# Performance work log

Hardware: AMD Instinct MI355X
Metric: run time of the kernel (lower is better)

The kernel has to match this reference:

```python
import jax, jax.numpy as jnp
import numpy as np

NUM_ITERS = 3

def squash(t, axis):
    # scale = |t|^2/(1+|t|^2); out = scale * t / |t|
    sn = jnp.sum(t * t, axis=axis, keepdims=True)
    return (sn / (1.0 + sn)) * t / jnp.sqrt(sn)


def setup_inputs() -> dict:
    key = jax.random.key(0)
    k1, k2, k3, k4 = jax.random.split(key, 4)
    B = 128
    inputs = jax.random.normal(k1, (B, 256, 20, 20), dtype=jnp.float32)
    conv_w = jax.random.normal(k2, (8, 32, 256, 9, 9), dtype=jnp.float32) * 0.05
    conv_b = jax.random.normal(k3, (8, 32), dtype=jnp.float32) * 0.05
    route_weights = jax.random.normal(k4, (10, 1152, 8, 16), dtype=jnp.float32)
    return {"inputs": inputs, "conv_w": conv_w, "conv_b": conv_b,
            "route_weights": route_weights}


def reference(inputs, conv_w, conv_b, route_weights):
    B = inputs.shape[0]
    K, O, Cin, kh, kw = conv_w.shape          # 8 capsules, 32 out-chans each
    # --- primary capsules: 8 parallel convs fused into one grouped-output conv ---
    w = conv_w.reshape(K * O, Cin, kh, kw)
    out = jax.lax.conv_general_dilated(
        inputs, w, window_strides=(2, 2), padding='VALID',
        dimension_numbers=('NCHW', 'OIHW', 'NCHW'))  # [B, K*O, 6, 6]
    out = out + conv_b.reshape(K * O)[None, :, None, None]
    H = out.shape[-1]
    x = out.reshape(B, K, O * H * H).transpose(0, 2, 1)  # [B, 1152, 8]
    x = squash(x, axis=2)
    # --- routing layer ---
    # prediction_vectors: x[None,:,:,None,:] @ W[:,None,:,:,:] -> [10,B,1152,1,16]
    pred = jnp.einsum('bri,crio->cbro', x, route_weights)[:, :, :, None, :]
    logits = jnp.zeros_like(pred)
    v = None
    for i in range(NUM_ITERS):
        # routing_softmax(dim=2): softmax over the routes axis (faithful to source)
        c = jax.nn.softmax(logits, axis=2)
        s = jnp.sum(c * pred, axis=2, keepdims=True)  # [10,B,1,1,16]
        v = squash(s, axis=1)                          # squash default dim=1 (batch) -- faithful
        if i != NUM_ITERS - 1:
            logits = logits + jnp.sum(pred * v, axis=-1, keepdims=True)
    # [10,B,1,1,16] -> squeeze -> [10,B,16] -> permute(1,0,2) -> [B,10,16]
    return jnp.squeeze(v).transpose(1, 0, 2)
```

## Files before the change

kernel.cpp:

```cpp
#include <hip/hip_runtime.h>
#include <math.h>

typedef _Float16 f16;
typedef _Float16 f16x4 __attribute__((ext_vector_type(4)));
typedef _Float16 f16x8 __attribute__((ext_vector_type(8)));
typedef float f32x4 __attribute__((ext_vector_type(4)));
typedef float f32x8 __attribute__((ext_vector_type(8)));

#define AS1 __attribute__((address_space(1)))
#define AS3 __attribute__((address_space(3)))

__device__ __forceinline__ void gld_lds16(const f16* g, f16* l) {
#if defined(__has_builtin) && __has_builtin(__builtin_amdgcn_global_load_lds)
    __builtin_amdgcn_global_load_lds((const AS1 void*)g, (AS3 void*)l, 16, 0, 0);
#else
    *(uint4*)l = *(const uint4*)g;
#endif
}

__global__ __launch_bounds__(256) void transpose_input(
    const float* __restrict__ inp, f16* __restrict__ out)
{
    const int b = blockIdx.x, c0 = blockIdx.y * 32, p0 = blockIdx.z * 32;
    const int tx = threadIdx.x, ty = threadIdx.y;
    __shared__ float t[32][33];
#pragma unroll
    for (int j = 0; j < 4; ++j) {
        int c = ty + j * 8, p = p0 + tx;
        if (p < 400) t[c][tx] = inp[((size_t)b * 256 + c0 + c) * 400 + p];
    }
    __syncthreads();
#pragma unroll
    for (int j = 0; j < 4; ++j) {
        int p = p0 + ty + j * 8;
        if (p < 400) out[((size_t)b * 400 + p) * 256 + c0 + tx] = (f16)t[tx][ty + j * 8];
    }
}

__global__ __launch_bounds__(256) void permute_w(
    const float* __restrict__ cw, f16* __restrict__ w_t)
{
    const int n = blockIdx.x, t = threadIdx.x;
    __shared__ f16 buf[81 * 258];
    const float* src = cw + (size_t)n * 20736;
    for (int i = t; i < 20736; i += 256) {
        int cin = i / 81, p = i - cin * 81;
        buf[p * 258 + cin] = (f16)src[i];
    }
    __syncthreads();
    f16* dst = w_t + (size_t)n * 20736;
    for (int j = t; j < 20736; j += 256) {
        int p = j >> 8, cin = j & 255;
        dst[j] = buf[p * 258 + cin];
    }
}

__global__ __launch_bounds__(256) void permute_rw(
    const float* __restrict__ rw, f16* __restrict__ rwh)
{
    int g = blockIdx.x * 256 + threadIdx.x;
    int cr = g >> 5, rem = g & 31;
    int o = rem >> 1, h = (rem & 1) * 4;
    const float* src = rw + (size_t)cr * 128 + o;
    f16x4 v;
#pragma unroll
    for (int j = 0; j < 4; ++j) v[j] = (f16)src[(h + j) * 16];
    *(f16x4*)(rwh + (size_t)cr * 128 + o * 8 + h) = v;
}

#define SPLITK 14
__global__ __launch_bounds__(256, 2) void conv_mfma(
    const f16* __restrict__ in_t,
    const f16* __restrict__ w_t,
    f16* __restrict__ part)
{
    __shared__ f16 As[3][128 * 32];
    __shared__ f16 Bs[3][256 * 32];
    const int tid = threadIdx.x;
    const int lane = tid & 63, wave = tid >> 6;
    const int wm = wave >> 1, wn = wave & 1;

    const int bid = blockIdx.x + 36 * blockIdx.z;
    const int wgid = (bid & 7) * 63 + (bid >> 3);
    const int m0 = (wgid % 36) * 128;
    const int kz = wgid / 36;

    const int kc0 = kz * 46 + (kz < 4 ? kz : 4);
    const int NT  = (kz < 4) ? 47 : 46;

    int srcA[2], srcB[4];
#pragma unroll
    for (int i = 0; i < 2; ++i) {
        int pairp = i * 32 + (tid >> 3);
        int chunk8 = (tid & 7) ^ (pairp & 7);
        int e = chunk8 >> 2, q4 = chunk8 & 3;
        int m = m0 + pairp * 2 + e;
        int b = m / 36, hw = m - b * 36;
        int ho = hw / 6, wo = hw - ho * 6;
        srcA[i] = ((b * 20 + 2 * ho) * 20 + 2 * wo) * 256 + q4 * 8;
    }
#pragma unroll
    for (int i = 0; i < 4; ++i) {
        int pairp = i * 32 + (tid >> 3);
        int chunk8 = (tid & 7) ^ (pairp & 7);
        int e = chunk8 >> 2, q4 = chunk8 & 3;
        int n = pairp * 2 + e;
        srcB[i] = n * 20736 + q4 * 8;
    }

    const int row = lane & 15, quad = lane >> 4;
    int offA[4], offB[8];
#pragma unroll
    for (int mt = 0; mt < 4; ++mt) {
        int m = wm * 64 + mt * 16 + row;
        int ph8 = (((m & 1) << 2) + quad) ^ ((m >> 1) & 7);
        offA[mt] = (m >> 1) * 64 + ph8 * 8;
    }
#pragma unroll
    for (int nt = 0; nt < 8; ++nt) {
        int n = wn * 128 + nt * 16 + row;
        int ph8 = (((n & 1) << 2) + quad) ^ ((n >> 1) & 7);
        offB[nt] = (n >> 1) * 64 + ph8 * 8;
    }

    f32x4 acc[4][8] = {};

#define KOFFS(T) int kc = kc0 + (T); int pp = kc >> 3, cq = kc & 7;           \
    int kh = pp / 9, kw = pp - kh * 9;                                        \
    int koffA = (kh * 20 + kw) * 256 + cq * 32; int koffB = kc * 32;
#define STAGE1(T, BUF) do { KOFFS(T)                                          \
        gld_lds16(in_t + srcA[0] + koffA, &As[BUF][tid * 8]);                 \
        gld_lds16(in_t + srcA[1] + koffA, &As[BUF][2048 + tid * 8]);          \
        gld_lds16(w_t + srcB[0] + koffB, &Bs[BUF][tid * 8]);                  \
    } while (0)
#define STAGE2(T, BUF) do { KOFFS(T)                                          \
        gld_lds16(w_t + srcB[1] + koffB, &Bs[BUF][2048 + tid * 8]);           \
        gld_lds16(w_t + srcB[2] + koffB, &Bs[BUF][4096 + tid * 8]);           \
        gld_lds16(w_t + srcB[3] + koffB, &Bs[BUF][6144 + tid * 8]);           \
    } while (0)

    STAGE1(0, 0); STAGE2(0, 0);
    STAGE1(1, 1); STAGE2(1, 1);
    asm volatile("s_waitcnt vmcnt(6)" ::: "memory");
    __builtin_amdgcn_s_barrier();

    int buf = 0;
    for (int t = 0; t < NT; ++t) {
        const f16* Ab = &As[buf][0];
        const f16* Bb = &Bs[buf][0];
        int bn = buf + 2; if (bn >= 3) bn -= 3;
        f16x8 af[4], bfr[8];

#pragma unroll
        for (int mt = 0; mt < 4; ++mt) af[mt] = *(const f16x8*)(Ab + offA[mt]);
#pragma unroll
        for (int nt = 0; nt < 4; ++nt) bfr[nt] = *(const f16x8*)(Bb + offB[nt]);
        if (t + 2 < NT) STAGE1(t + 2, bn);
        __builtin_amdgcn_s_barrier();
        asm volatile("s_waitcnt lgkmcnt(0)" ::: "memory");
        __builtin_amdgcn_sched_barrier(0);
        __builtin_amdgcn_s_setprio(1);
#pragma unroll
        for (int mt = 0; mt < 4; ++mt)
#pragma unroll
            for (int nt = 0; nt < 4; ++nt)
                acc[mt][nt] = __builtin_amdgcn_mfma_f32_16x16x32_f16(
                    af[mt], bfr[nt], acc[mt][nt], 0, 0, 0);
        __builtin_amdgcn_s_setprio(0);
        __builtin_amdgcn_s_barrier();

#pragma unroll
        for (int nt = 4; nt < 8; ++nt) bfr[nt] = *(const f16x8*)(Bb + offB[nt]);
        if (t + 2 < NT) STAGE2(t + 2, bn);
        if (t + 2 < NT)
            asm volatile("s_waitcnt vmcnt(6)" ::: "memory");
        else if (t + 1 < NT)
            asm volatile("s_waitcnt vmcnt(0)" ::: "memory");
        __builtin_amdgcn_s_barrier();
        asm volatile("s_waitcnt lgkmcnt(0)" ::: "memory");
        __builtin_amdgcn_sched_barrier(0);
        __builtin_amdgcn_s_setprio(1);
#pragma unroll
        for (int mt = 0; mt < 4; ++mt)
#pragma unroll
            for (int nt = 4; nt < 8; ++nt)
                acc[mt][nt] = __builtin_amdgcn_mfma_f32_16x16x32_f16(
                    af[mt], bfr[nt], acc[mt][nt], 0, 0, 0);
        __builtin_amdgcn_s_setprio(0);
        __builtin_amdgcn_s_barrier();

        if (++buf == 3) buf = 0;
    }
#undef STAGE1
#undef STAGE2
#undef KOFFS

    const int col = lane & 15, qr = (lane >> 4) * 4;
    f16* pb = part + (size_t)kz * 4608 * 256;
#pragma unroll
    for (int mt = 0; mt < 4; ++mt)
#pragma unroll
        for (int rg = 0; rg < 4; ++rg) {
            int m = m0 + wm * 64 + mt * 16 + qr + rg;
#pragma unroll
            for (int nt = 0; nt < 8; ++nt) {
                int n = wn * 128 + nt * 16 + col;
                pb[(size_t)m * 256 + n] = (f16)acc[mt][nt][rg];
            }
        }
}

__global__ __launch_bounds__(256) void combine_squash(
    const f16* __restrict__ part, const float* __restrict__ bias,
    f16* __restrict__ xh)
{
    int idx = blockIdx.x * 256 + threadIdx.x;
    int m = idx >> 3, g = idx & 7;
    int b = m / 36, hw = m - b * 36;
    float val[8][4];
#pragma unroll
    for (int k = 0; k < 8; ++k)
#pragma unroll
        for (int j = 0; j < 4; ++j) val[k][j] = bias[k * 32 + g * 4 + j];
#pragma unroll
    for (int s = 0; s < SPLITK; ++s) {
        const f16* p = part + ((size_t)s * 4608 + m) * 256 + g * 4;
#pragma unroll
        for (int k = 0; k < 8; ++k) {
            f16x4 v = *(const f16x4*)(p + k * 32);
#pragma unroll
            for (int j = 0; j < 4; ++j) val[k][j] += (float)v[j];
        }
    }
#pragma unroll
    for (int j = 0; j < 4; ++j) {
        float sn = 0.f;
#pragma unroll
        for (int k = 0; k < 8; ++k) sn += val[k][j] * val[k][j];
        float scale = sqrtf(sn) / (1.f + sn);
        int r = (g * 4 + j) * 36 + hw;
        f16x8 hv;
#pragma unroll
        for (int k = 0; k < 8; ++k) hv[k] = (f16)(val[k][j] * scale);
        *(f16x8*)(xh + ((size_t)b * 1152 + r) * 8) = hv;
    }
}

__global__ __launch_bounds__(256) void pred_s0h(
    const f16* __restrict__ xh,
    const f16* __restrict__ rwh,
    f16* __restrict__ pred,
    float* __restrict__ s0)
{
    const int c = blockIdx.x, r0 = blockIdx.y * 32, b0 = blockIdx.z * 32;
    const int tid = threadIdx.x;
    const int o = tid & 15, rp = tid >> 4;
    const int r = r0 + rp * 2;

    __shared__ float s_sh[32 * 16];
    s_sh[tid] = 0.f; s_sh[tid + 256] = 0.f;

    f16x8 w0h = *(const f16x8*)(rwh + ((size_t)(c * 1152 + r) * 16 + o) * 8);
    f16x8 w1h = *(const f16x8*)(rwh + ((size_t)(c * 1152 + r + 1) * 16 + o) * 8);
    f32x8 W0 = __builtin_convertvector(w0h, f32x8);
    f32x8 W1 = __builtin_convertvector(w1h, f32x8);
    __syncthreads();

    for (int bb = 0; bb < 32; ++bb) {
        const int b = b0 + bb;
        f16x8 x0h = *(const f16x8*)(xh + ((size_t)b * 1152 + r) * 8);
        f16x8 x1h = *(const f16x8*)(xh + ((size_t)b * 1152 + r + 1) * 8);
        f32x8 X0 = __builtin_convertvector(x0h, f32x8);
        f32x8 X1 = __builtin_convertvector(x1h, f32x8);
        float p0 = X0[0]*W0[0] + X0[1]*W0[1] + X0[2]*W0[2] + X0[3]*W0[3]
                 + X0[4]*W0[4] + X0[5]*W0[5] + X0[6]*W0[6] + X0[7]*W0[7];
        float p1 = X1[0]*W1[0] + X1[1]*W1[1] + X1[2]*W1[2] + X1[3]*W1[3]
                 + X1[4]*W1[4] + X1[5]*W1[5] + X1[6]*W1[6] + X1[7]*W1[7];
        f16* pb = pred + ((size_t)(c * 128 + b) * 1152 + r) * 16 + o;
        pb[0]  = (f16)p0;
        pb[16] = (f16)p1;
        float ps = p0 + p1;
        ps += __shfl_xor(ps, 16);
        ps += __shfl_xor(ps, 32);
        if ((tid & 63) < 16) atomicAdd(&s_sh[bb * 16 + o], ps);
    }
    __syncthreads();
    for (int i = tid; i < 512; i += 256) {
        int bb = i >> 4, oo = i & 15;
        atomicAdd(&s0[((size_t)c * 128 + b0 + bb) * 16 + oo], s_sh[i]);
    }
}

__global__ __launch_bounds__(256) void route_f16v(
    const f16* __restrict__ pred,
    const float* __restrict__ sa, const float* __restrict__ za,
    const float* __restrict__ sb2, const float* __restrict__ zb2,
    float* __restrict__ s_out,
    float* __restrict__ z_out)
{
    const int c = blockIdx.x, b = blockIdx.y, tid = threadIdx.x;
    const size_t base = (size_t)(c * 128 + b) * 1152;
    const int o = tid & 15, seg = tid >> 4;

    __shared__ float lred[16][17];
    __shared__ float vs[16];

#define VSADD(S, Z) do {                                                      \
        float part_ = 0.f;                                                    \
        _Pragma("unroll")                                                     \
        for (int j = 0; j < 8; ++j) {                                         \
            int bb = seg * 8 + j;                                             \
            float zin = (Z) ? 1.f / (Z)[c * 128 + bb] : (1.f / 1152.f);       \
            float q = (S)[((size_t)c * 128 + bb) * 16 + o] * zin;             \
            part_ += q * q;                                                   \
        }                                                                     \
        lred[seg][o] = part_;                                                 \
        __syncthreads();                                                      \
        if (tid < 16) {                                                       \
            float t_ = 0.f;                                                   \
            _Pragma("unroll")                                                 \
            for (int i = 0; i < 16; ++i) t_ += lred[i][tid];                  \
            float zin = (Z) ? 1.f / (Z)[c * 128 + b] : (1.f / 1152.f);        \
            vs[tid] += (S)[((size_t)c * 128 + b) * 16 + tid] * zin *          \
                       sqrtf(t_) / (1.f + t_);                                \
        }                                                                     \
        __syncthreads();                                                      \
    } while (0)

    if (tid < 16) vs[tid] = 0.f;
    __syncthreads();
    VSADD(sa, za);
    if (sb2) VSADD(sb2, zb2);
#undef VSADD

    float vr[16];
#pragma unroll
    for (int j = 0; j < 16; ++j) vr[j] = vs[j];

    float sacc[16];
#pragma unroll
    for (int j = 0; j < 16; ++j) sacc[j] = 0.f;
    float zacc = 0.f;

    for (int r = tid; r < 1152; r += 256) {
        const f16x8* pp = (const f16x8*)(pred + (base + r) * 16);
        f32x8 q0 = __builtin_convertvector(pp[0], f32x8);
        f32x8 q1 = __builtin_convertvector(pp[1], f32x8);
        float t = 0.f;
#pragma unroll
        for (int j = 0; j < 8; ++j) t += q0[j] * vr[j] + q1[j] * vr[j + 8];
        float e = __expf(t);
#pragma unroll
        for (int j = 0; j < 8; ++j) { sacc[j] += e * q0[j]; sacc[j + 8] += e * q1[j]; }
        zacc += e;
    }

    __shared__ float red[256][16];
    __shared__ float red2[16][16];
    __shared__ float zred[256];
    __shared__ float zpart[16];
#pragma unroll
    for (int j = 0; j < 16; ++j) red[tid][j] = sacc[j];
    zred[tid] = zacc;
    __syncthreads();
    {
        float t = 0.f;
#pragma unroll
        for (int j = 0; j < 16; ++j) t += red[seg * 16 + j][o];
        red2[seg][o] = t;
        if (tid < 16) {
            float tz = 0.f;
#pragma unroll
            for (int j = 0; j < 16; ++j) tz += zred[tid * 16 + j];
            zpart[tid] = tz;
        }
    }
    __syncthreads();
    if (tid < 16) {
        float t = 0.f;
#pragma unroll
        for (int sg = 0; sg < 16; ++sg) t += red2[sg][tid];
        s_out[(size_t)(c * 128 + b) * 16 + tid] = t;
    } else if (tid == 16) {
        float tz = 0.f;
#pragma unroll
        for (int j = 0; j < 16; ++j) tz += zpart[j];
        z_out[c * 128 + b] = tz;
    }
}

__global__ __launch_bounds__(128) void squash_final(
    const float* __restrict__ s, const float* __restrict__ z,
    float* __restrict__ out)
{
    const int c = blockIdx.x, b = threadIdx.x;
    float sv[16];
    const float* sp = s + ((size_t)c * 128 + b) * 16;
    float zin = 1.f / z[c * 128 + b];
#pragma unroll
    for (int o = 0; o < 16; ++o) sv[o] = sp[o] * zin;
    __shared__ float m[16][129];
#pragma unroll
    for (int o = 0; o < 16; ++o) m[o][b] = sv[o] * sv[o];
    __syncthreads();
    __shared__ float sn[16];
    if (b < 16) {
        float t = 0.f;
        for (int i = 0; i < 128; ++i) t += m[b][i];
        sn[b] = t;
    }
    __syncthreads();
#pragma unroll
    for (int o = 0; o < 16; ++o) {
        float scale = sqrtf(sn[o]) / (1.f + sn[o]);
        out[((size_t)b * 10 + c) * 16 + o] = sv[o] * scale;
    }
}

extern "C" void kernel_launch(void* const* d_in, const int* in_sizes, int n_in,
                              void* d_out, int out_size, void* d_ws, size_t ws_size,
                              hipStream_t stream)
{
    (void)in_sizes; (void)n_in; (void)out_size; (void)ws_size;
    const float* inp = (const float*)d_in[0];
    const float* cw  = (const float*)d_in[1];
    const float* cb  = (const float*)d_in[2];
    const float* rw  = (const float*)d_in[3];
    float* out = (float*)d_out;

    char* ws = (char*)d_ws;
    f16*   part = (f16*)(ws);
    f16*   pred = (f16*)(ws);
    f16*   in_t = (f16*)(ws + 33030144);
    f16*   w_t  = (f16*)(ws + 59244544);
    f16*   rwh  = (f16*)(ws + 69861376);
    f16*   xh   = (f16*)(ws + 72810496);
    float* s0   = (float*)(ws + 75169792);
    float* sB   = (float*)(ws + 75251712);
    float* sC   = (float*)(ws + 75333632);
    float* zB   = (float*)(ws + 75415552);
    float* zC   = (float*)(ws + 75420672);

    hipMemsetAsync(s0, 0, 81920, stream);

    transpose_input<<<dim3(128, 8, 13), dim3(32, 8), 0, stream>>>(inp, in_t);
    permute_w<<<256, 256, 0, stream>>>(cw, w_t);
    permute_rw<<<1440, 256, 0, stream>>>(rw, rwh);
    conv_mfma<<<dim3(36, 1, SPLITK), 256, 0, stream>>>(in_t, w_t, part);
    combine_squash<<<144, 256, 0, stream>>>(part, cb, xh);

    pred_s0h<<<dim3(10, 36, 4), 256, 0, stream>>>(xh, rwh, pred, s0);

    route_f16v<<<dim3(10, 128), 256, 0, stream>>>(pred, s0, nullptr, nullptr, nullptr,
                                                  sB, zB);
    route_f16v<<<dim3(10, 128), 256, 0, stream>>>(pred, s0, nullptr, sB, zB,
                                                  sC, zC);
    squash_final<<<10, 128, 0, stream>>>(sC, zC, out);
}
```

Baseline: 241.0 us.

## Merge preprocessing kernels and memset into one launch, parallelize split-K combine

```diff
diff --git a/kernel.cpp b/kernel.cpp
--- a/kernel.cpp
+++ b/kernel.cpp
@@ -18,54 +18,57 @@
 #endif
 }
 
-__global__ __launch_bounds__(256) void transpose_input(
-    const float* __restrict__ inp, f16* __restrict__ out)
-{
-    const int b = blockIdx.x, c0 = blockIdx.y * 32, p0 = blockIdx.z * 32;
-    const int tx = threadIdx.x, ty = threadIdx.y;
-    __shared__ float t[32][33];
-#pragma unroll
-    for (int j = 0; j < 4; ++j) {
-        int c = ty + j * 8, p = p0 + tx;
-        if (p < 400) t[c][tx] = inp[((size_t)b * 256 + c0 + c) * 400 + p];
-    }
-    __syncthreads();
-#pragma unroll
-    for (int j = 0; j < 4; ++j) {
-        int p = p0 + ty + j * 8;
-        if (p < 400) out[((size_t)b * 400 + p) * 256 + c0 + tx] = (f16)t[tx][ty + j * 8];
-    }
-}
-
-__global__ __launch_bounds__(256) void permute_w(
-    const float* __restrict__ cw, f16* __restrict__ w_t)
-{
-    const int n = blockIdx.x, t = threadIdx.x;
-    __shared__ f16 buf[81 * 258];
-    const float* src = cw + (size_t)n * 20736;
-    for (int i = t; i < 20736; i += 256) {
-        int cin = i / 81, p = i - cin * 81;
-        buf[p * 258 + cin] = (f16)src[i];
-    }
-    __syncthreads();
-    f16* dst = w_t + (size_t)n * 20736;
-    for (int j = t; j < 20736; j += 256) {
-        int p = j >> 8, cin = j & 255;
-        dst[j] = buf[p * 258 + cin];
-    }
-}
-
-__global__ __launch_bounds__(256) void permute_rw(
-    const float* __restrict__ rw, f16* __restrict__ rwh)
-{
-    int g = blockIdx.x * 256 + threadIdx.x;
-    int cr = g >> 5, rem = g & 31;
-    int o = rem >> 1, h = (rem & 1) * 4;
-    const float* src = rw + (size_t)cr * 128 + o;
-    f16x4 v;
-#pragma unroll
-    for (int j = 0; j < 4; ++j) v[j] = (f16)src[(h + j) * 16];
-    *(f16x4*)(rwh + (size_t)cr * 128 + o * 8 + h) = v;
+__global__ __launch_bounds__(256) void mega_pre(
+    const float* __restrict__ inp, f16* __restrict__ in_t,
+    const float* __restrict__ cw,  f16* __restrict__ w_t,
+    const float* __restrict__ rw,  f16* __restrict__ rwh,
+    float* __restrict__ s0)
+{
+    __shared__ __align__(16) char smem[81 * 258 * 2];
+    const int bx = blockIdx.x, tid = threadIdx.x;
+
+    if (bx < 13312) {
+        const int b = bx & 127, c0 = ((bx >> 7) & 7) * 32, p0 = (bx >> 10) * 32;
+        const int tx = tid & 31, ty = tid >> 5;
+        float (*t)[33] = (float(*)[33])smem;
+#pragma unroll
+        for (int j = 0; j < 4; ++j) {
+            int c = ty + j * 8, p = p0 + tx;
+            if (p < 400) t[c][tx] = inp[((size_t)b * 256 + c0 + c) * 400 + p];
+        }
+        __syncthreads();
+#pragma unroll
+        for (int j = 0; j < 4; ++j) {
+            int p = p0 + ty + j * 8;
+            if (p < 400) in_t[((size_t)b * 400 + p) * 256 + c0 + tx] = (f16)t[tx][ty + j * 8];
+        }
+    } else if (bx < 13568) {
+        const int n = bx - 13312;
+        f16* buf = (f16*)smem;
+        const float* src = cw + (size_t)n * 20736;
+        for (int i = tid; i < 20736; i += 256) {
+            int cin = i / 81, p = i - cin * 81;
+            buf[p * 258 + cin] = (f16)src[i];
+        }
+        __syncthreads();
+        f16* dst = w_t + (size_t)n * 20736;
+        for (int j = tid; j < 20736; j += 256) {
+            int p = j >> 8, cin = j & 255;
+            dst[j] = buf[p * 258 + cin];
+        }
+    } else if (bx < 15008) {
+        int g = (bx - 13568) * 256 + tid;
+        int cr = g >> 5, rem = g & 31;
+        int o = rem >> 1, h = (rem & 1) * 4;
+        const float* src = rw + (size_t)cr * 128 + o;
+        f16x4 v;
+#pragma unroll
+        for (int j = 0; j < 4; ++j) v[j] = (f16)src[(h + j) * 16];
+        *(f16x4*)(rwh + (size_t)cr * 128 + o * 8 + h) = v;
+    } else {
+        int idx = (bx - 15008) * 256 + tid;
+        ((float4*)s0)[idx] = make_float4(0.f, 0.f, 0.f, 0.f);
+    }
 }
 
 #define SPLITK 14
@@ -210,21 +213,18 @@
         }
 }
 
-__global__ __launch_bounds__(256) void combine_squash(
+__global__ __launch_bounds__(256) void combine_squash4(
     const f16* __restrict__ part, const float* __restrict__ bias,
     f16* __restrict__ xh)
 {
     int idx = blockIdx.x * 256 + threadIdx.x;
-    int m = idx >> 3, g = idx & 7;
+    int g = idx & 7, si = (idx >> 3) & 3, m = idx >> 5;
     int b = m / 36, hw = m - b * 36;
-    float val[8][4];
-#pragma unroll
-    for (int k = 0; k < 8; ++k)
-#pragma unroll
-        for (int j = 0; j < 4; ++j) val[k][j] = bias[k * 32 + g * 4 + j];
-#pragma unroll
-    for (int s = 0; s < SPLITK; ++s) {
-        const f16* p = part + ((size_t)s * 4608 + m) * 256 + g * 4;
+    int sbeg = si * 4, scnt = (si < 3) ? 4 : 2;
+
+    float val[8][4] = {};
+    for (int s2 = 0; s2 < scnt; ++s2) {
+        const f16* p = part + ((size_t)(sbeg + s2) * 4608 + m) * 256 + g * 4;
 #pragma unroll
         for (int k = 0; k < 8; ++k) {
             f16x4 v = *(const f16x4*)(p + k * 32);
@@ -233,16 +233,29 @@
         }
     }
 #pragma unroll
-    for (int j = 0; j < 4; ++j) {
-        float sn = 0.f;
-#pragma unroll
-        for (int k = 0; k < 8; ++k) sn += val[k][j] * val[k][j];
-        float scale = sqrtf(sn) / (1.f + sn);
-        int r = (g * 4 + j) * 36 + hw;
-        f16x8 hv;
-#pragma unroll
-        for (int k = 0; k < 8; ++k) hv[k] = (f16)(val[k][j] * scale);
-        *(f16x8*)(xh + ((size_t)b * 1152 + r) * 8) = hv;
+    for (int k = 0; k < 8; ++k)
+#pragma unroll
+        for (int j = 0; j < 4; ++j) {
+            val[k][j] += __shfl_xor(val[k][j], 8);
+            val[k][j] += __shfl_xor(val[k][j], 16);
+        }
+    if (si == 0) {
+#pragma unroll
+        for (int j = 0; j < 4; ++j) {
+            float sn = 0.f;
+            float vb[8];
+#pragma unroll
+            for (int k = 0; k < 8; ++k) {
+                vb[k] = val[k][j] + bias[k * 32 + g * 4 + j];
+                sn += vb[k] * vb[k];
+            }
+            float scale = sqrtf(sn) / (1.f + sn);
+            int r = (g * 4 + j) * 36 + hw;
+            f16x8 hv;
+#pragma unroll
+            for (int k = 0; k < 8; ++k) hv[k] = (f16)(vb[k] * scale);
+            *(f16x8*)(xh + ((size_t)b * 1152 + r) * 8) = hv;
+        }
     }
 }
 
@@ -266,23 +279,35 @@
     f32x8 W1 = __builtin_convertvector(w1h, f32x8);
     __syncthreads();
 
-    for (int bb = 0; bb < 32; ++bb) {
-        const int b = b0 + bb;
-        f16x8 x0h = *(const f16x8*)(xh + ((size_t)b * 1152 + r) * 8);
-        f16x8 x1h = *(const f16x8*)(xh + ((size_t)b * 1152 + r + 1) * 8);
-        f32x8 X0 = __builtin_convertvector(x0h, f32x8);
-        f32x8 X1 = __builtin_convertvector(x1h, f32x8);
-        float p0 = X0[0]*W0[0] + X0[1]*W0[1] + X0[2]*W0[2] + X0[3]*W0[3]
-                 + X0[4]*W0[4] + X0[5]*W0[5] + X0[6]*W0[6] + X0[7]*W0[7];
-        float p1 = X1[0]*W1[0] + X1[1]*W1[1] + X1[2]*W1[2] + X1[3]*W1[3]
-                 + X1[4]*W1[4] + X1[5]*W1[5] + X1[6]*W1[6] + X1[7]*W1[7];
-        f16* pb = pred + ((size_t)(c * 128 + b) * 1152 + r) * 16 + o;
-        pb[0]  = (f16)p0;
-        pb[16] = (f16)p1;
-        float ps = p0 + p1;
-        ps += __shfl_xor(ps, 16);
-        ps += __shfl_xor(ps, 32);
-        if ((tid & 63) < 16) atomicAdd(&s_sh[bb * 16 + o], ps);
+    for (int bb = 0; bb < 32; bb += 2) {
+        const int ba = b0 + bb, bc = b0 + bb + 1;
+        f16x8 xa0 = *(const f16x8*)(xh + ((size_t)ba * 1152 + r) * 8);
+        f16x8 xa1 = *(const f16x8*)(xh + ((size_t)ba * 1152 + r + 1) * 8);
+        f16x8 xc0 = *(const f16x8*)(xh + ((size_t)bc * 1152 + r) * 8);
+        f16x8 xc1 = *(const f16x8*)(xh + ((size_t)bc * 1152 + r + 1) * 8);
+        f32x8 A0 = __builtin_convertvector(xa0, f32x8);
+        f32x8 A1 = __builtin_convertvector(xa1, f32x8);
+        f32x8 C0 = __builtin_convertvector(xc0, f32x8);
+        f32x8 C1 = __builtin_convertvector(xc1, f32x8);
+        float pa0 = A0[0]*W0[0] + A0[1]*W0[1] + A0[2]*W0[2] + A0[3]*W0[3]
+                  + A0[4]*W0[4] + A0[5]*W0[5] + A0[6]*W0[6] + A0[7]*W0[7];
+        float pa1 = A1[0]*W1[0] + A1[1]*W1[1] + A1[2]*W1[2] + A1[3]*W1[3]
+                  + A1[4]*W1[4] + A1[5]*W1[5] + A1[6]*W1[6] + A1[7]*W1[7];
+        float pc0 = C0[0]*W0[0] + C0[1]*W0[1] + C0[2]*W0[2] + C0[3]*W0[3]
+                  + C0[4]*W0[4] + C0[5]*W0[5] + C0[6]*W0[6] + C0[7]*W0[7];
+        float pc1 = C1[0]*W1[0] + C1[1]*W1[1] + C1[2]*W1[2] + C1[3]*W1[3]
+                  + C1[4]*W1[4] + C1[5]*W1[5] + C1[6]*W1[6] + C1[7]*W1[7];
+        f16* pba = pred + ((size_t)(c * 128 + ba) * 1152 + r) * 16 + o;
+        f16* pbc = pred + ((size_t)(c * 128 + bc) * 1152 + r) * 16 + o;
+        pba[0]  = (f16)pa0;  pba[16] = (f16)pa1;
+        pbc[0]  = (f16)pc0;  pbc[16] = (f16)pc1;
+        float psa = pa0 + pa1, psc = pc0 + pc1;
+        psa += __shfl_xor(psa, 16); psc += __shfl_xor(psc, 16);
+        psa += __shfl_xor(psa, 32); psc += __shfl_xor(psc, 32);
+        if ((tid & 63) < 16) {
+            atomicAdd(&s_sh[bb * 16 + o], psa);
+            atomicAdd(&s_sh[(bb + 1) * 16 + o], psc);
+        }
     }
     __syncthreads();
     for (int i = tid; i < 512; i += 256) {
@@ -441,13 +466,10 @@
     float* zB   = (float*)(ws + 75415552);
     float* zC   = (float*)(ws + 75420672);
 
-    hipMemsetAsync(s0, 0, 81920, stream);
-
-    transpose_input<<<dim3(128, 8, 13), dim3(32, 8), 0, stream>>>(inp, in_t);
-    permute_w<<<256, 256, 0, stream>>>(cw, w_t);
-    permute_rw<<<1440, 256, 0, stream>>>(rw, rwh);
+    mega_pre<<<15028, 256, 0, stream>>>(inp, in_t, cw, w_t, rw, rwh, s0);
+
     conv_mfma<<<dim3(36, 1, SPLITK), 256, 0, stream>>>(in_t, w_t, part);
-    combine_squash<<<144, 256, 0, stream>>>(part, cb, xh);
+    combine_squash4<<<576, 256, 0, stream>>>(part, cb, xh);
 
     pred_s0h<<<dim3(10, 36, 4), 256, 0, stream>>>(xh, rwh, pred, s0);
 
```

After: 253.1 us. +5.0%, slower.
